# Optimization experiments

Hardware: AMD Instinct MI355X
Metric: run time of the kernel (lower is better)

Reference implementation:

```python
import jax, jax.numpy as jnp
import numpy as np

N_NODES = 50000
N_EDGES = 800000
IN_C, HID_C, OUT_C = 128, 96, 64
BN_EPS = 1e-5


def setup_inputs() -> dict:
    key = jax.random.key(0)
    ks = jax.random.split(key, 12)
    x = jax.random.normal(ks[0], (N_NODES, IN_C), dtype=jnp.float32)
    edge_weight = jax.random.uniform(ks[1], (N_EDGES,), dtype=jnp.float32)
    row = jax.random.randint(ks[2], (N_EDGES,), 0, N_NODES, dtype=jnp.int32)
    col = jax.random.randint(ks[3], (N_EDGES,), 0, N_NODES, dtype=jnp.int32)
    s = 0.05
    W1 = jax.random.normal(ks[4], (IN_C, HID_C), dtype=jnp.float32) * s
    b1 = jnp.zeros((HID_C,), dtype=jnp.float32)
    W2 = jax.random.normal(ks[5], (HID_C, HID_C), dtype=jnp.float32) * s
    b2 = jnp.zeros((HID_C,), dtype=jnp.float32)
    W3 = jax.random.normal(ks[6], (HID_C, OUT_C), dtype=jnp.float32) * s
    b3 = jnp.zeros((OUT_C,), dtype=jnp.float32)
    g1 = jnp.ones((HID_C,), dtype=jnp.float32)
    be1 = jnp.zeros((HID_C,), dtype=jnp.float32)
    g2 = jnp.ones((HID_C,), dtype=jnp.float32)
    be2 = jnp.zeros((HID_C,), dtype=jnp.float32)
    return {"x": x, "edge_weight": edge_weight, "row": row, "col": col,
            "W1": W1, "b1": b1, "W2": W2, "b2": b2, "W3": W3, "b3": b3,
            "g1": g1, "be1": be1, "g2": g2, "be2": be2}


def _gcn_conv(h, edge_weight, row, col, W, b):
    # GCNConv: adj_norm @ (h @ W) + b, adj in COO with normalized edge_weight
    h = h @ W  # [N, d_out]
    msg = edge_weight[:, None] * h[col]  # gather + scale: [E, d_out]
    agg = jax.ops.segment_sum(msg, row, num_segments=N_NODES)  # scatter-add
    return agg + b


def _batch_norm(h, gamma, beta):
    # BatchNorm1d (training-mode batch statistics, biased variance)
    mean = jnp.mean(h, axis=0)
    var = jnp.var(h, axis=0)
    return (h - mean) * jax.lax.rsqrt(var + BN_EPS) * gamma + beta


def reference(x, edge_weight, row, col, W1, b1, W2, b2, W3, b3, g1, be1, g2, be2):
    h = _gcn_conv(x, edge_weight, row, col, W1, b1)
    h = jax.nn.relu(_batch_norm(h, g1, be1))  # dropout is identity in eval
    h = _gcn_conv(h, edge_weight, row, col, W2, b2)
    h = jax.nn.relu(_batch_norm(h, g2, be2))
    h = _gcn_conv(h, edge_weight, row, col, W3, b3)
    return jax.nn.log_softmax(h, axis=-1)
```

## Files before the change

kernel.cpp:

```cpp
#include <hip/hip_runtime.h>
#include <hip/hip_bf16.h>
#include <math.h>

#define N_NODES 50000
#define N_EDGES 800000
#define IN_C 128
#define HID_C 96
#define OUT_C 64
#define BN_EPS 1e-5f

#define ELL_SHIFT 6
#define ELL_CAP   64

#define NGRP 8
#define GRP_ROWS ((N_NODES + NGRP - 1) / NGRP)

#define EW_SCALE 65535.0f
#define EW_INV   (1.0f / 65535.0f)

typedef __attribute__((ext_vector_type(8))) short short8;
typedef __attribute__((ext_vector_type(4))) float f32x4;

static __device__ __forceinline__ unsigned short f2b(float f) {
    __hip_bfloat16 b = __float2bfloat16(f);
    return *reinterpret_cast<unsigned short*>(&b);
}
static __device__ __forceinline__ float b2f(unsigned short u) {
    return __uint_as_float((unsigned)u << 16);
}

__global__ void prep_all(const float* __restrict__ W1, const float* __restrict__ W2,
                         const float* __restrict__ W3,
                         unsigned short* __restrict__ Wt1,
                         unsigned short* __restrict__ Wt2,
                         unsigned short* __restrict__ Wt3,
                         int* __restrict__ cnt, float* __restrict__ stats) {
    int i = blockIdx.x * blockDim.x + threadIdx.x;
    const int n1 = IN_C * HID_C, n2 = HID_C * HID_C, n3 = HID_C * OUT_C;
    if (i < n1) {
        int j = i / IN_C, k = i % IN_C;
        Wt1[i] = f2b(W1[k * HID_C + j]);
    } else if (i < n1 + n2) {
        int t = i - n1, j = t / HID_C, k = t % HID_C;
        Wt2[t] = f2b(W2[k * HID_C + j]);
    } else if (i < n1 + n2 + n3) {
        int t = i - n1 - n2, j = t / HID_C, k = t % HID_C;
        Wt3[t] = f2b(W3[k * OUT_C + j]);
    }
    if (i < N_NODES) cnt[i] = 0;
    if (i < 4 * HID_C) stats[i] = 0.f;
}

__global__ __launch_bounds__(256)
void fill_ell(const int* __restrict__ row, const int* __restrict__ col,
              const float* __restrict__ ew, int* __restrict__ cnt,
              unsigned int* __restrict__ pairs) {
    int g = blockIdx.x & (NGRP - 1);
    int e = (blockIdx.x >> 3) * 256 + threadIdx.x;
    if (e >= N_EDGES) return;
    int r = row[e];
    int lo = g * GRP_ROWS;
    if ((unsigned)(r - lo) >= (unsigned)GRP_ROWS) return;
    int slot = atomicAdd(&cnt[r], 1);
    if (slot < ELL_CAP) {
        unsigned wq = (unsigned)(ew[e] * EW_SCALE + 0.5f);
        pairs[((size_t)r << ELL_SHIFT) + slot] =
            (wq << 16) | (unsigned)col[e];
    }
}

template <int K, int J, bool APPLY, bool XBF16>
__global__ __launch_bounds__(256)
void gemm_mfma(const void* __restrict__ xin,
               const unsigned short* __restrict__ Wt,
               const float* __restrict__ stats,
               const float* __restrict__ gamma,
               const float* __restrict__ beta,
               unsigned short* __restrict__ h, int N) {
    constexpr int MT = 64;
    constexpr int SK = K + 8;
    constexpr int NT = J / 16;
    __shared__ unsigned short Xs[MT * SK];
    __shared__ unsigned short Ws[J * SK];
    __shared__ float scsh_s[APPLY ? 2 * K : 2];

    int tid = threadIdx.x;
    int tileBase = blockIdx.x * MT;

    if (APPLY) {
        if (tid < K) {
            const float invN = 1.f / N_NODES;
            float mean = stats[tid] * invN;
            float var = stats[K + tid] * invN - mean * mean;
            float sc = gamma[tid] * rsqrtf(var + BN_EPS);
            scsh_s[tid] = sc;
            scsh_s[K + tid] = beta[tid] - mean * sc;
        }
        __syncthreads();
    }

    if (XBF16) {
        const unsigned short* xb = (const unsigned short*)xin;
        for (int i = tid; i < MT * (K / 8); i += 256) {
            int node = i / (K / 8), kq = i % (K / 8);
            int gn = min(tileBase + node, N - 1);
            const unsigned short* src = xb + (size_t)gn * K + kq * 8;
            ushort4 u0 = *(const ushort4*)(src);
            ushort4 u1 = *(const ushort4*)(src + 4);
            if (APPLY) {
                int kb = kq * 8;
                float v0 = fmaxf(b2f(u0.x) * scsh_s[kb + 0] + scsh_s[K + kb + 0], 0.f);
                float v1 = fmaxf(b2f(u0.y) * scsh_s[kb + 1] + scsh_s[K + kb + 1], 0.f);
                float v2 = fmaxf(b2f(u0.z) * scsh_s[kb + 2] + scsh_s[K + kb + 2], 0.f);
                float v3 = fmaxf(b2f(u0.w) * scsh_s[kb + 3] + scsh_s[K + kb + 3], 0.f);
                float v4 = fmaxf(b2f(u1.x) * scsh_s[kb + 4] + scsh_s[K + kb + 4], 0.f);
                float v5 = fmaxf(b2f(u1.y) * scsh_s[kb + 5] + scsh_s[K + kb + 5], 0.f);
                float v6 = fmaxf(b2f(u1.z) * scsh_s[kb + 6] + scsh_s[K + kb + 6], 0.f);
                float v7 = fmaxf(b2f(u1.w) * scsh_s[kb + 7] + scsh_s[K + kb + 7], 0.f);
                u0 = make_ushort4(f2b(v0), f2b(v1), f2b(v2), f2b(v3));
                u1 = make_ushort4(f2b(v4), f2b(v5), f2b(v6), f2b(v7));
            }
            *(ushort4*)&Xs[node * SK + kq * 8] = u0;
            *(ushort4*)&Xs[node * SK + kq * 8 + 4] = u1;
        }
    } else {
        const float* xf = (const float*)xin;
        for (int i = tid; i < MT * (K / 4); i += 256) {
            int node = i / (K / 4), kq = i % (K / 4);
            int gn = min(tileBase + node, N - 1);
            float4 v = *(const float4*)(xf + (size_t)gn * K + kq * 4);
            ushort4 o = make_ushort4(f2b(v.x), f2b(v.y), f2b(v.z), f2b(v.w));
            *(ushort4*)&Xs[node * SK + kq * 4] = o;
        }
    }
    for (int i = tid; i < J * (K / 4); i += 256) {
        int j = i / (K / 4), kq = i % (K / 4);
        *(ushort4*)&Ws[j * SK + kq * 4] =
            *(const ushort4*)(Wt + (size_t)j * K + kq * 4);
    }
    __syncthreads();

    int lane = tid & 63;
    int w = tid >> 6;
    int m16 = lane & 15;
    int quad = lane >> 4;

    f32x4 acc[NT];
#pragma unroll
    for (int nt = 0; nt < NT; ++nt) acc[nt] = (f32x4){0.f, 0.f, 0.f, 0.f};

    const unsigned short* xrow = &Xs[(w * 16 + m16) * SK];
#pragma unroll
    for (int k0 = 0; k0 < K; k0 += 32) {
        short8 a = *(const short8*)(xrow + k0 + quad * 8);
#pragma unroll
        for (int nt = 0; nt < NT; ++nt) {
            short8 b = *(const short8*)&Ws[(nt * 16 + m16) * SK + k0 + quad * 8];
            acc[nt] = __builtin_amdgcn_mfma_f32_16x16x32_bf16(a, b, acc[nt], 0, 0, 0);
        }
    }

#pragma unroll
    for (int nt = 0; nt < NT; ++nt) {
#pragma unroll
        for (int r = 0; r < 4; ++r) {
            int node = tileBase + w * 16 + quad * 4 + r;
            if (node < N)
                h[(size_t)node * J + nt * 16 + m16] = f2b(acc[nt][r]);
        }
    }
}

template <int D, bool LSM>
__global__ void agg_ell_kernel(const unsigned short* __restrict__ h,
                               const int* __restrict__ cnt,
                               const unsigned int* __restrict__ pairs,
                               unsigned short* __restrict__ outb,
                               float* __restrict__ outf,
                               const float* __restrict__ b3) {
    constexpr int G = D / 4;
    int t = blockIdx.x * blockDim.x + threadIdx.x;
    if (t >= N_NODES * G) return;
    int n = t / G, g = t % G;
    int end = min(cnt[n], ELL_CAP);
    const unsigned int* ep = pairs + ((size_t)n << ELL_SHIFT);
    float4 acc = make_float4(0.f, 0.f, 0.f, 0.f);
    float4 acc2 = make_float4(0.f, 0.f, 0.f, 0.f);
    int i = 0;
    for (; i + 3 < end; i += 4) {
        uint4 p = *(const uint4*)(ep + i);
        ushort4 u0 = *(const ushort4*)(h + (size_t)(p.x & 0xFFFFu) * D + g * 4);
        ushort4 u1 = *(const ushort4*)(h + (size_t)(p.y & 0xFFFFu) * D + g * 4);
        ushort4 u2 = *(const ushort4*)(h + (size_t)(p.z & 0xFFFFu) * D + g * 4);
        ushort4 u3 = *(const ushort4*)(h + (size_t)(p.w & 0xFFFFu) * D + g * 4);
        float w0 = (float)(p.x >> 16) * EW_INV;
        float w1 = (float)(p.y >> 16) * EW_INV;
        float w2 = (float)(p.z >> 16) * EW_INV;
        float w3 = (float)(p.w >> 16) * EW_INV;
        acc.x += w0 * b2f(u0.x); acc.y += w0 * b2f(u0.y);
        acc.z += w0 * b2f(u0.z); acc.w += w0 * b2f(u0.w);
        acc2.x += w1 * b2f(u1.x); acc2.y += w1 * b2f(u1.y);
        acc2.z += w1 * b2f(u1.z); acc2.w += w1 * b2f(u1.w);
        acc.x += w2 * b2f(u2.x); acc.y += w2 * b2f(u2.y);
        acc.z += w2 * b2f(u2.z); acc.w += w2 * b2f(u2.w);
        acc2.x += w3 * b2f(u3.x); acc2.y += w3 * b2f(u3.y);
        acc2.z += w3 * b2f(u3.z); acc2.w += w3 * b2f(u3.w);
    }
    for (; i < end; ++i) {
        unsigned p = ep[i];
        float w = (float)(p >> 16) * EW_INV;
        ushort4 u = *(const ushort4*)(h + (size_t)(p & 0xFFFFu) * D + g * 4);
        acc.x += w * b2f(u.x); acc.y += w * b2f(u.y);
        acc.z += w * b2f(u.z); acc.w += w * b2f(u.w);
    }
    acc.x += acc2.x; acc.y += acc2.y; acc.z += acc2.z; acc.w += acc2.w;

    if (LSM) {
        float4 bv = *(const float4*)(b3 + g * 4);
        float4 v = make_float4(acc.x + bv.x, acc.y + bv.y,
                               acc.z + bv.z, acc.w + bv.w);
        float m = fmaxf(fmaxf(v.x, v.y), fmaxf(v.z, v.w));
#pragma unroll
        for (int mask = 1; mask < 16; mask <<= 1)
            m = fmaxf(m, __shfl_xor(m, mask, 16));
        float s = expf(v.x - m) + expf(v.y - m) + expf(v.z - m) + expf(v.w - m);
#pragma unroll
        for (int mask = 1; mask < 16; mask <<= 1)
            s += __shfl_xor(s, mask, 16);
        float l = m + logf(s);
        *(float4*)(outf + (size_t)n * D + g * 4) =
            make_float4(v.x - l, v.y - l, v.z - l, v.w - l);
    } else {
        ushort4 o = make_ushort4(f2b(acc.x), f2b(acc.y), f2b(acc.z), f2b(acc.w));
        *(ushort4*)(outb + (size_t)n * D + g * 4) = o;
    }
}

#define STATS_BLOCKS 250

template <int D>
__global__ void bn_stats_kernel(const unsigned short* __restrict__ a,
                                float* __restrict__ sums, int N) {
    constexpr int G = D / 4;
    constexpr int ROWS = 384 / G;
    int t = threadIdx.x;
    int g = t % G, r0 = t / G;
    float4 s4 = make_float4(0.f, 0.f, 0.f, 0.f);
    float4 q4 = make_float4(0.f, 0.f, 0.f, 0.f);
    for (int r = blockIdx.x * ROWS + r0; r < N; r += gridDim.x * ROWS) {
        ushort4 u = *(const ushort4*)(a + (size_t)r * D + g * 4);
        float vx = b2f(u.x), vy = b2f(u.y), vz = b2f(u.z), vw = b2f(u.w);
        s4.x += vx; s4.y += vy; s4.z += vz; s4.w += vw;
        q4.x += vx * vx; q4.y += vy * vy; q4.z += vz * vz; q4.w += vw * vw;
    }
    __shared__ __align__(16) float sh[2 * ROWS * D];
    *(float4*)&sh[r0 * D + g * 4] = s4;
    *(float4*)&sh[ROWS * D + r0 * D + g * 4] = q4;
    __syncthreads();
    if (t < D) {
        float s0 = 0.f, s1 = 0.f;
#pragma unroll
        for (int k = 0; k < ROWS; ++k) {
            s0 += sh[k * D + t];
            s1 += sh[ROWS * D + k * D + t];
        }
        atomicAdd(&sums[t], s0);
        atomicAdd(&sums[D + t], s1);
    }
}

extern "C" void kernel_launch(void* const* d_in, const int* in_sizes, int n_in,
                              void* d_out, int out_size, void* d_ws, size_t ws_size,
                              hipStream_t stream) {
    const float* x   = (const float*)d_in[0];
    const float* ew  = (const float*)d_in[1];
    const int*   row = (const int*)d_in[2];
    const int*   col = (const int*)d_in[3];
    const float* W1  = (const float*)d_in[4];
    const float* W2  = (const float*)d_in[6];
    const float* W3  = (const float*)d_in[8];
    const float* b3  = (const float*)d_in[9];
    const float* g1  = (const float*)d_in[10];
    const float* be1 = (const float*)d_in[11];
    const float* g2  = (const float*)d_in[12];
    const float* be2 = (const float*)d_in[13];
    float* out = (float*)d_out;

    unsigned short* B      = (unsigned short*)d_ws;
    unsigned short* A      = B + (size_t)N_NODES * HID_C;
    unsigned short* Wt1    = A + (size_t)N_NODES * HID_C;
    unsigned short* Wt2    = Wt1 + IN_C * HID_C;
    unsigned short* Wt3    = Wt2 + HID_C * HID_C;
    unsigned int*   pairs  = (unsigned int*)(Wt3 + HID_C * OUT_C);
    int*            cnt    = (int*)(pairs + ((size_t)N_NODES << ELL_SHIFT));
    float*          stats1 = (float*)(cnt + N_NODES);
    float*          stats2 = stats1 + 2 * HID_C;

    const int T = 256;
    const int gridE   = (N_EDGES + T - 1) / T;
    const int gridA96 = (N_NODES * (HID_C / 4) + T - 1) / T;
    const int gridA64 = (N_NODES * (OUT_C / 4) + T - 1) / T;
    const int gridG   = (N_NODES + 63) / 64;
    const int gridP   = (N_NODES + T - 1) / T;

    prep_all<<<gridP, T, 0, stream>>>(W1, W2, W3, Wt1, Wt2, Wt3, cnt, stats1);
    fill_ell<<<gridE * NGRP, T, 0, stream>>>(row, col, ew, cnt, pairs);

    gemm_mfma<IN_C, HID_C, false, false><<<gridG, T, 0, stream>>>(
        x, Wt1, nullptr, nullptr, nullptr, A, N_NODES);
    agg_ell_kernel<HID_C, false><<<gridA96, T, 0, stream>>>(
        A, cnt, pairs, B, nullptr, nullptr);
    bn_stats_kernel<HID_C><<<STATS_BLOCKS, 384, 0, stream>>>(B, stats1, N_NODES);

    gemm_mfma<HID_C, HID_C, true, true><<<gridG, T, 0, stream>>>(
        B, Wt2, stats1, g1, be1, A, N_NODES);
    agg_ell_kernel<HID_C, false><<<gridA96, T, 0, stream>>>(
        A, cnt, pairs, B, nullptr, nullptr);
    bn_stats_kernel<HID_C><<<STATS_BLOCKS, 384, 0, stream>>>(B, stats2, N_NODES);

    gemm_mfma<HID_C, OUT_C, true, true><<<gridG, T, 0, stream>>>(
        B, Wt3, stats2, g2, be2, A, N_NODES);
    agg_ell_kernel<OUT_C, true><<<gridA64, T, 0, stream>>>(
        A, cnt, pairs, nullptr, out, b3);
}
```

Measured before the change: 270.2 us.

## Fuse BatchNorm statistics into ELL aggregation with 4 threads per node

Replaces the separate aggregation and bn_stats kernels with one aggregation kernel that also reduces per-channel sum and sum of squares. It uses wave shuffles and shared memory, then atomically adds into one of 4 sliced stat buffers to reduce atomic contention. Each node is now handled by 4 threads that each cover a quarter of the channels with 16-byte gathers, instead of one thread per 4 channels. This removes a full re-read of the aggregated activations and two kernel launches. The cost is more registers per thread and fewer threads issuing gathers, with stats now computed from bf16-rounded values.

```diff
diff --git a/kernel.cpp b/kernel.cpp
--- a/kernel.cpp
+++ b/kernel.cpp
@@ -18,6 +18,8 @@
 #define EW_SCALE 65535.0f
 #define EW_INV   (1.0f / 65535.0f)
 
+#define ST_SLICES 4
+
 typedef __attribute__((ext_vector_type(8))) short short8;
 typedef __attribute__((ext_vector_type(4))) float f32x4;
 
@@ -28,6 +30,19 @@
 static __device__ __forceinline__ float b2f(unsigned short u) {
     return __uint_as_float((unsigned)u << 16);
 }
+static __device__ __forceinline__ unsigned pack2(float a, float b) {
+    return (unsigned)f2b(a) | ((unsigned)f2b(b) << 16);
+}
+
+#define FMA8(B, V, W)                                          \
+    acc[(B) + 0] += (W) * __uint_as_float((V).x << 16);        \
+    acc[(B) + 1] += (W) * __uint_as_float((V).x & 0xffff0000u);\
+    acc[(B) + 2] += (W) * __uint_as_float((V).y << 16);        \
+    acc[(B) + 3] += (W) * __uint_as_float((V).y & 0xffff0000u);\
+    acc[(B) + 4] += (W) * __uint_as_float((V).z << 16);        \
+    acc[(B) + 5] += (W) * __uint_as_float((V).z & 0xffff0000u);\
+    acc[(B) + 6] += (W) * __uint_as_float((V).w << 16);        \
+    acc[(B) + 7] += (W) * __uint_as_float((V).w & 0xffff0000u);
 
 __global__ void prep_all(const float* __restrict__ W1, const float* __restrict__ W2,
                          const float* __restrict__ W3,
@@ -48,7 +63,7 @@
         Wt3[t] = f2b(W3[k * OUT_C + j]);
     }
     if (i < N_NODES) cnt[i] = 0;
-    if (i < 4 * HID_C) stats[i] = 0.f;
+    if (i < 2 * ST_SLICES * 2 * HID_C) stats[i] = 0.f;
 }
 
 __global__ __launch_bounds__(256)
@@ -89,9 +104,15 @@
 
     if (APPLY) {
         if (tid < K) {
+            float s = 0.f, sq = 0.f;
+#pragma unroll
+            for (int sl = 0; sl < ST_SLICES; ++sl) {
+                s  += stats[sl * 2 * K + tid];
+                sq += stats[sl * 2 * K + K + tid];
+            }
             const float invN = 1.f / N_NODES;
-            float mean = stats[tid] * invN;
-            float var = stats[K + tid] * invN - mean * mean;
+            float mean = s * invN;
+            float var = sq * invN - mean * mean;
             float sc = gamma[tid] * rsqrtf(var + BN_EPS);
             scsh_s[tid] = sc;
             scsh_s[K + tid] = beta[tid] - mean * sc;
@@ -171,101 +192,130 @@
     }
 }
 
-template <int D, bool LSM>
-__global__ void agg_ell_kernel(const unsigned short* __restrict__ h,
-                               const int* __restrict__ cnt,
-                               const unsigned int* __restrict__ pairs,
-                               unsigned short* __restrict__ outb,
-                               float* __restrict__ outf,
-                               const float* __restrict__ b3) {
-    constexpr int G = D / 4;
-    int t = blockIdx.x * blockDim.x + threadIdx.x;
-    if (t >= N_NODES * G) return;
-    int n = t / G, g = t % G;
-    int end = min(cnt[n], ELL_CAP);
-    const unsigned int* ep = pairs + ((size_t)n << ELL_SHIFT);
-    float4 acc = make_float4(0.f, 0.f, 0.f, 0.f);
-    float4 acc2 = make_float4(0.f, 0.f, 0.f, 0.f);
+template <int D, bool LSM, bool STATS>
+__global__ __launch_bounds__(256)
+void agg_fused(const unsigned short* __restrict__ h,
+               const int* __restrict__ cnt,
+               const unsigned int* __restrict__ pairs,
+               unsigned short* __restrict__ outb,
+               float* __restrict__ outf,
+               const float* __restrict__ b3,
+               float* __restrict__ stats) {
+    constexpr int TPN = 4;
+    constexpr int C = D / TPN;
+    constexpr int NPB = 256 / TPN;
+    __shared__ float shS[STATS ? 16 * C : 1];
+    __shared__ float shQ[STATS ? 16 * C : 1];
+
+    int tid = threadIdx.x;
+    int q = tid & 3;
+    int nloc = tid >> 2;
+    int n = blockIdx.x * NPB + nloc;
+    bool valid = n < N_NODES;
+    int nn = valid ? n : N_NODES - 1;
+    int end = valid ? min(cnt[nn], ELL_CAP) : 0;
+    const unsigned* ep = pairs + ((size_t)nn << ELL_SHIFT);
+    const int cbase = q * C;
+
+    float acc[C];
+#pragma unroll
+    for (int c = 0; c < C; ++c) acc[c] = 0.f;
+
     int i = 0;
-    for (; i + 3 < end; i += 4) {
-        uint4 p = *(const uint4*)(ep + i);
-        ushort4 u0 = *(const ushort4*)(h + (size_t)(p.x & 0xFFFFu) * D + g * 4);
-        ushort4 u1 = *(const ushort4*)(h + (size_t)(p.y & 0xFFFFu) * D + g * 4);
-        ushort4 u2 = *(const ushort4*)(h + (size_t)(p.z & 0xFFFFu) * D + g * 4);
-        ushort4 u3 = *(const ushort4*)(h + (size_t)(p.w & 0xFFFFu) * D + g * 4);
-        float w0 = (float)(p.x >> 16) * EW_INV;
-        float w1 = (float)(p.y >> 16) * EW_INV;
-        float w2 = (float)(p.z >> 16) * EW_INV;
-        float w3 = (float)(p.w >> 16) * EW_INV;
-        acc.x += w0 * b2f(u0.x); acc.y += w0 * b2f(u0.y);
-        acc.z += w0 * b2f(u0.z); acc.w += w0 * b2f(u0.w);
-        acc2.x += w1 * b2f(u1.x); acc2.y += w1 * b2f(u1.y);
-        acc2.z += w1 * b2f(u1.z); acc2.w += w1 * b2f(u1.w);
-        acc.x += w2 * b2f(u2.x); acc.y += w2 * b2f(u2.y);
-        acc.z += w2 * b2f(u2.z); acc.w += w2 * b2f(u2.w);
-        acc2.x += w3 * b2f(u3.x); acc2.y += w3 * b2f(u3.y);
-        acc2.z += w3 * b2f(u3.z); acc2.w += w3 * b2f(u3.w);
-    }
-    for (; i < end; ++i) {
-        unsigned p = ep[i];
-        float w = (float)(p >> 16) * EW_INV;
-        ushort4 u = *(const ushort4*)(h + (size_t)(p & 0xFFFFu) * D + g * 4);
-        acc.x += w * b2f(u.x); acc.y += w * b2f(u.y);
-        acc.z += w * b2f(u.z); acc.w += w * b2f(u.w);
-    }
-    acc.x += acc2.x; acc.y += acc2.y; acc.z += acc2.z; acc.w += acc2.w;
+    for (; i + 1 < end; i += 2) {
+        unsigned p0 = ep[i], p1 = ep[i + 1];
+        float w0 = (float)(p0 >> 16) * EW_INV;
+        float w1 = (float)(p1 >> 16) * EW_INV;
+        const unsigned short* r0 = h + (size_t)(p0 & 0xFFFFu) * D + cbase;
+        const unsigned short* r1 = h + (size_t)(p1 & 0xFFFFu) * D + cbase;
+        uint4 v0[C / 8], v1[C / 8];
+#pragma unroll
+        for (int ch = 0; ch < C / 8; ++ch) v0[ch] = *(const uint4*)(r0 + ch * 8);
+#pragma unroll
+        for (int ch = 0; ch < C / 8; ++ch) v1[ch] = *(const uint4*)(r1 + ch * 8);
+#pragma unroll
+        for (int ch = 0; ch < C / 8; ++ch) { FMA8(ch * 8, v0[ch], w0) }
+#pragma unroll
+        for (int ch = 0; ch < C / 8; ++ch) { FMA8(ch * 8, v1[ch], w1) }
+    }
+    if (i < end) {
+        unsigned p0 = ep[i];
+        float w0 = (float)(p0 >> 16) * EW_INV;
+        const unsigned short* r0 = h + (size_t)(p0 & 0xFFFFu) * D + cbase;
+#pragma unroll
+        for (int ch = 0; ch < C / 8; ++ch) {
+            uint4 v = *(const uint4*)(r0 + ch * 8);
+            FMA8(ch * 8, v, w0)
+        }
+    }
 
     if (LSM) {
-        float4 bv = *(const float4*)(b3 + g * 4);
-        float4 v = make_float4(acc.x + bv.x, acc.y + bv.y,
-                               acc.z + bv.z, acc.w + bv.w);
-        float m = fmaxf(fmaxf(v.x, v.y), fmaxf(v.z, v.w));
-#pragma unroll
-        for (int mask = 1; mask < 16; mask <<= 1)
-            m = fmaxf(m, __shfl_xor(m, mask, 16));
-        float s = expf(v.x - m) + expf(v.y - m) + expf(v.z - m) + expf(v.w - m);
-#pragma unroll
-        for (int mask = 1; mask < 16; mask <<= 1)
-            s += __shfl_xor(s, mask, 16);
+        float v[C];
+#pragma unroll
+        for (int c = 0; c < C; ++c) v[c] = acc[c] + b3[cbase + c];
+        float m = v[0];
+#pragma unroll
+        for (int c = 1; c < C; ++c) m = fmaxf(m, v[c]);
+        m = fmaxf(m, __shfl_xor(m, 1));
+        m = fmaxf(m, __shfl_xor(m, 2));
+        float s = 0.f;
+#pragma unroll
+        for (int c = 0; c < C; ++c) s += expf(v[c] - m);
+        s += __shfl_xor(s, 1);
+        s += __shfl_xor(s, 2);
         float l = m + logf(s);
-        *(float4*)(outf + (size_t)n * D + g * 4) =
-            make_float4(v.x - l, v.y - l, v.z - l, v.w - l);
+        if (valid) {
+#pragma unroll
+            for (int ch = 0; ch < C / 4; ++ch) {
+                float4 o = make_float4(v[ch * 4 + 0] - l, v[ch * 4 + 1] - l,
+                                       v[ch * 4 + 2] - l, v[ch * 4 + 3] - l);
+                *(float4*)(outf + (size_t)n * D + cbase + ch * 4) = o;
+            }
+        }
     } else {
-        ushort4 o = make_ushort4(f2b(acc.x), f2b(acc.y), f2b(acc.z), f2b(acc.w));
-        *(ushort4*)(outb + (size_t)n * D + g * 4) = o;
-    }
-}
-
-#define STATS_BLOCKS 250
-
-template <int D>
-__global__ void bn_stats_kernel(const unsigned short* __restrict__ a,
-                                float* __restrict__ sums, int N) {
-    constexpr int G = D / 4;
-    constexpr int ROWS = 384 / G;
-    int t = threadIdx.x;
-    int g = t % G, r0 = t / G;
-    float4 s4 = make_float4(0.f, 0.f, 0.f, 0.f);
-    float4 q4 = make_float4(0.f, 0.f, 0.f, 0.f);
-    for (int r = blockIdx.x * ROWS + r0; r < N; r += gridDim.x * ROWS) {
-        ushort4 u = *(const ushort4*)(a + (size_t)r * D + g * 4);
-        float vx = b2f(u.x), vy = b2f(u.y), vz = b2f(u.z), vw = b2f(u.w);
-        s4.x += vx; s4.y += vy; s4.z += vz; s4.w += vw;
-        q4.x += vx * vx; q4.y += vy * vy; q4.z += vz * vz; q4.w += vw * vw;
-    }
-    __shared__ __align__(16) float sh[2 * ROWS * D];
-    *(float4*)&sh[r0 * D + g * 4] = s4;
-    *(float4*)&sh[ROWS * D + r0 * D + g * 4] = q4;
-    __syncthreads();
-    if (t < D) {
-        float s0 = 0.f, s1 = 0.f;
-#pragma unroll
-        for (int k = 0; k < ROWS; ++k) {
-            s0 += sh[k * D + t];
-            s1 += sh[ROWS * D + k * D + t];
-        }
-        atomicAdd(&sums[t], s0);
-        atomicAdd(&sums[D + t], s1);
+#pragma unroll
+        for (int c = 0; c < C; ++c) acc[c] = b2f(f2b(acc[c]));
+#pragma unroll
+        for (int ch = 0; ch < C / 8; ++ch) {
+            uint4 o;
+            o.x = pack2(acc[ch * 8 + 0], acc[ch * 8 + 1]);
+            o.y = pack2(acc[ch * 8 + 2], acc[ch * 8 + 3]);
+            o.z = pack2(acc[ch * 8 + 4], acc[ch * 8 + 5]);
+            o.w = pack2(acc[ch * 8 + 6], acc[ch * 8 + 7]);
+            if (valid)
+                *(uint4*)(outb + (size_t)n * D + cbase + ch * 8) = o;
+        }
+        if (STATS) {
+            int lane = tid & 63;
+            int wv = tid >> 6;
+#pragma unroll
+            for (int c = 0; c < C; ++c) {
+                float s = acc[c];
+                float sq = s * s;
+#pragma unroll
+                for (int msk = 4; msk < 64; msk <<= 1) {
+                    s  += __shfl_xor(s, msk);
+                    sq += __shfl_xor(sq, msk);
+                }
+                if (lane < 4) {
+                    shS[(wv * 4 + lane) * C + c] = s;
+                    shQ[(wv * 4 + lane) * C + c] = sq;
+                }
+            }
+            __syncthreads();
+            if (tid < D) {
+                int qq = tid / C, cl = tid % C;
+                float S = 0.f, Q = 0.f;
+#pragma unroll
+                for (int w2 = 0; w2 < 4; ++w2) {
+                    S += shS[(w2 * 4 + qq) * C + cl];
+                    Q += shQ[(w2 * 4 + qq) * C + cl];
+                }
+                int slice = blockIdx.x & (ST_SLICES - 1);
+                atomicAdd(&stats[slice * 2 * D + tid], S);
+                atomicAdd(&stats[slice * 2 * D + D + tid], Q);
+            }
+        }
     }
 }
 
@@ -294,32 +344,28 @@
     unsigned int*   pairs  = (unsigned int*)(Wt3 + HID_C * OUT_C);
     int*            cnt    = (int*)(pairs + ((size_t)N_NODES << ELL_SHIFT));
     float*          stats1 = (float*)(cnt + N_NODES);
-    float*          stats2 = stats1 + 2 * HID_C;
+    float*          stats2 = stats1 + ST_SLICES * 2 * HID_C;
 
     const int T = 256;
-    const int gridE   = (N_EDGES + T - 1) / T;
-    const int gridA96 = (N_NODES * (HID_C / 4) + T - 1) / T;
-    const int gridA64 = (N_NODES * (OUT_C / 4) + T - 1) / T;
-    const int gridG   = (N_NODES + 63) / 64;
-    const int gridP   = (N_NODES + T - 1) / T;
+    const int gridE  = (N_EDGES + T - 1) / T;
+    const int gridG  = (N_NODES + 63) / 64;
+    const int gridP  = (N_NODES + T - 1) / T;
 
     prep_all<<<gridP, T, 0, stream>>>(W1, W2, W3, Wt1, Wt2, Wt3, cnt, stats1);
     fill_ell<<<gridE * NGRP, T, 0, stream>>>(row, col, ew, cnt, pairs);
 
     gemm_mfma<IN_C, HID_C, false, false><<<gridG, T, 0, stream>>>(
         x, Wt1, nullptr, nullptr, nullptr, A, N_NODES);
-    agg_ell_kernel<HID_C, false><<<gridA96, T, 0, stream>>>(
-        A, cnt, pairs, B, nullptr, nullptr);
-    bn_stats_kernel<HID_C><<<STATS_BLOCKS, 384, 0, stream>>>(B, stats1, N_NODES);
+    agg_fused<HID_C, false, true><<<gridG, T, 0, stream>>>(
+        A, cnt, pairs, B, nullptr, nullptr, stats1);
 
     gemm_mfma<HID_C, HID_C, true, true><<<gridG, T, 0, stream>>>(
         B, Wt2, stats1, g1, be1, A, N_NODES);
-    agg_ell_kernel<HID_C, false><<<gridA96, T, 0, stream>>>(
-        A, cnt, pairs, B, nullptr, nullptr);
-    bn_stats_kernel<HID_C><<<STATS_BLOCKS, 384, 0, stream>>>(B, stats2, N_NODES);
+    agg_fused<HID_C, false, true><<<gridG, T, 0, stream>>>(
+        A, cnt, pairs, B, nullptr, nullptr, stats2);
 
     gemm_mfma<HID_C, OUT_C, true, true><<<gridG, T, 0, stream>>>(
         B, Wt3, stats2, g2, be2, A, N_NODES);
-    agg_ell_kernel<OUT_C, true><<<gridA64, T, 0, stream>>>(
-        A, cnt, pairs, nullptr, out, b3);
-}
+    agg_fused<OUT_C, true, false><<<gridG, T, 0, stream>>>(
+        A, cnt, pairs, nullptr, out, b3, nullptr);
+}
```

Measured after the change: 266.2 us. About the same (-1.5%).
